# Optimization experiments

Hardware: AMD Instinct MI355X
Metric: run time of the kernel (lower is better)

## Reference

```python
import jax, jax.numpy as jnp
import numpy as np

EPSILON = 0.05
SINKHORN_ITERS = 3
TEMP = 0.1
PROB_RATIO = 1.0
LAMBD = 15.0
MU = 1.0
NU = 1.0
GAMMA = 0.2

B, D, K = 16384, 512, 2048


def setup_inputs() -> dict:
    key = jax.random.key(0)
    k1, k2, k3 = jax.random.split(key, 3)
    z_1 = jax.random.normal(k1, (B, D), dtype=jnp.float32)
    z_2 = jax.random.normal(k2, (B, D), dtype=jnp.float32)
    W = jax.random.normal(k3, (K, D), dtype=jnp.float32) * (1.0 / np.sqrt(D))
    return {"z_1": z_1, "z_2": z_2, "W": W}


def _compute_v(z):
    # unbiased variance over batch dim, matching torch.var default
    var = jnp.var(z, axis=0, ddof=1)
    return jnp.mean(jnp.maximum(0.0, GAMMA - jnp.sqrt(var + 1e-8)))


def _compute_c(z):
    n, d = z.shape
    zc = z - jnp.mean(z, axis=0, keepdims=True)
    C = (zc.T @ zc) / (n - 1)  # [d, d] unbiased covariance (torch.cov)
    off = C - jnp.diag(jnp.diag(C))
    return jnp.sum(off * off) / d


def _l2norm(z):
    return z / jnp.clip(jnp.linalg.norm(z, axis=-1, keepdims=True), 1e-12)


def _sinkhorn(out):
    # out: [B, K] raw logits (no grad path)
    b, k = out.shape
    Q = jnp.exp(out / EPSILON).T  # [K, B]
    Q = Q / jnp.sum(Q)
    for _ in range(SINKHORN_ITERS):
        Q = Q / (jnp.sum(Q, axis=1, keepdims=True) * k)
        Q = Q / (jnp.sum(Q, axis=0, keepdims=True) * b)
    Q = Q * b
    return Q.T  # [B, K]


def reference(z_1, z_2, W):
    v_z1 = _compute_v(z_1)
    v_z2 = _compute_v(z_2)
    c_z1 = _compute_c(z_1)
    c_z2 = _compute_c(z_2)

    z1n = _l2norm(z_1)
    z2n = _l2norm(z_2)
    logits_1 = z1n @ W.T  # [B, K]
    logits_2 = z2n @ W.T

    tgt_w_1 = jax.lax.stop_gradient(logits_1 * PROB_RATIO + logits_2 * (1 - PROB_RATIO))
    tgt_w_2 = jax.lax.stop_gradient(logits_2 * PROB_RATIO + logits_1 * (1 - PROB_RATIO))
    tgt_probs_1 = _sinkhorn(tgt_w_1)
    tgt_probs_2 = _sinkhorn(tgt_w_2)

    l1 = logits_1 / TEMP
    l2 = logits_2 / TEMP
    lp1 = jax.nn.log_softmax(l1, axis=1)
    lp2 = jax.nn.log_softmax(l2, axis=1)

    loss_ce = -0.5 * (jnp.mean(jnp.sum(tgt_probs_1 * lp2, axis=1))
                      + jnp.mean(jnp.sum(tgt_probs_2 * lp1, axis=1)))
    loss_var = v_z1 + v_z2
    loss_cov = c_z1 + c_z2
    loss = LAMBD * loss_ce + MU * loss_var + NU * loss_cov

    # diagnostics (no-grad in original)
    logits = jnp.concatenate([l1, l2], axis=0)  # [2B, K]
    k_idx = jnp.argmax(logits, axis=-1)
    hard_probs = jnp.zeros((K,), logits.dtype).at[k_idx].add(1.0) / logits.shape[0]
    code_perplexity = jnp.exp(-jnp.sum(hard_probs * jnp.log(hard_probs + 1e-7)))
    avg_probs = jnp.mean(jax.nn.softmax(logits, axis=-1), axis=0)
    prob_perplexity = jnp.exp(-jnp.sum(avg_probs * jnp.log(avg_probs + 1e-7)))
    acc_1 = jnp.mean((jnp.argmax(l1, axis=1) == jnp.argmax(tgt_probs_2, axis=1)).astype(jnp.float32))
    acc_2 = jnp.mean((jnp.argmax(l2, axis=1) == jnp.argmax(tgt_probs_1, axis=1)).astype(jnp.float32))
    acc = 0.5 * (acc_1 + acc_2)

    return (loss, loss_ce, loss_var, loss_cov, code_perplexity, prob_perplexity, acc)
```

## Files before the change

### kernel.cpp

```cpp
#include <hip/hip_runtime.h>
#include <hip/hip_bf16.h>

#define B_N 16384
#define D_N 512
#define K_N 2048

typedef __attribute__((ext_vector_type(8))) short bf16x8;
typedef __attribute__((ext_vector_type(4))) float f32x4;
typedef __attribute__((ext_vector_type(4))) unsigned short u16x4;
typedef unsigned short u16;

__device__ __forceinline__ float bf2f(short s) {
  return __builtin_bit_cast(float, ((unsigned)(u16)s) << 16);
}
__device__ __forceinline__ u16 f2bf(float x) {
  return __builtin_bit_cast(u16, __float2bfloat16(x));
}
__device__ __forceinline__ float wred_sum(float v) {
#pragma unroll
  for (int o = 32; o; o >>= 1) v += __shfl_down(v, o, 64);
  return v;
}

__device__ __forceinline__ void gld16(const u16* g, const u16* l) {
  __builtin_amdgcn_global_load_lds((const __attribute__((address_space(1))) void*)g,
                                   (__attribute__((address_space(3))) void*)l, 16, 0, 0);
}

__global__ __launch_bounds__(256) void k_rownorm(const float* __restrict__ z1,
                                                 const float* __restrict__ z2,
                                                 u16* __restrict__ zn1, u16* __restrict__ zn2,
                                                 u16* __restrict__ zb1, u16* __restrict__ zb2) {
  int wid = threadIdx.x >> 6, lane = threadIdx.x & 63;
  int row = blockIdx.x * 4 + wid;
  const float* z; u16 *zn, *zb; int r;
  if (row < B_N) { z = z1; zn = zn1; zb = zb1; r = row; }
  else { z = z2; zn = zn2; zb = zb2; r = row - B_N; }
  const float4* zr = (const float4*)(z + (size_t)r * D_N);
  float4 va = zr[lane], vb = zr[lane + 64];
  float ss = va.x*va.x + va.y*va.y + va.z*va.z + va.w*va.w
           + vb.x*vb.x + vb.y*vb.y + vb.z*vb.z + vb.w*vb.w;
#pragma unroll
  for (int o = 32; o; o >>= 1) ss += __shfl_xor(ss, o, 64);
  float inv = 1.0f / fmaxf(sqrtf(ss), 1e-12f);
  u16x4 pa = {f2bf(va.x), f2bf(va.y), f2bf(va.z), f2bf(va.w)};
  u16x4 pb = {f2bf(vb.x), f2bf(vb.y), f2bf(vb.z), f2bf(vb.w)};
  u16x4 na = {f2bf(va.x*inv), f2bf(va.y*inv), f2bf(va.z*inv), f2bf(va.w*inv)};
  u16x4 nb = {f2bf(vb.x*inv), f2bf(vb.y*inv), f2bf(vb.z*inv), f2bf(vb.w*inv)};
  ((u16x4*)(zb + (size_t)r * D_N))[lane] = pa;
  ((u16x4*)(zb + (size_t)r * D_N))[lane + 64] = pb;
  ((u16x4*)(zn + (size_t)r * D_N))[lane] = na;
  ((u16x4*)(zn + (size_t)r * D_N))[lane + 64] = nb;
}

__global__ __launch_bounds__(256) void k_convW(const float* __restrict__ W,
                                               u16* __restrict__ Wb) {
  size_t base = ((size_t)blockIdx.x * 256 + threadIdx.x) * 8;
#pragma unroll
  for (int j = 0; j < 8; j++) Wb[base + j] = f2bf(W[base + j]);
}

__global__ __launch_bounds__(512) void k_colstats(const u16* __restrict__ zb1,
                                                  const u16* __restrict__ zb2,
                                                  float* __restrict__ csum,
                                                  float* __restrict__ csumsq) {
  int zi = blockIdx.z;
  const u16* z = zi ? zb2 : zb1;
  __shared__ float s1[512], s2[512];
  int t = threadIdx.y * 64 + threadIdx.x;
  s1[t] = 0.f; s2[t] = 0.f;
  __syncthreads();
  int c0 = threadIdx.x * 8;
  float a[8], a2[8];
#pragma unroll
  for (int e = 0; e < 8; e++) { a[e] = 0.f; a2[e] = 0.f; }
  for (int u = 0; u < 16; u++) {
    int r = blockIdx.y * 128 + threadIdx.y + 8 * u;
    bf16x8 v = *(const bf16x8*)&z[(size_t)r * D_N + c0];
#pragma unroll
    for (int e = 0; e < 8; e++) { float x = bf2f(v[e]); a[e] += x; a2[e] += x * x; }
  }
#pragma unroll
  for (int e = 0; e < 8; e++) {
    atomicAdd(&s1[c0 + e], a[e]);
    atomicAdd(&s2[c0 + e], a2[e]);
  }
  __syncthreads();
  atomicAdd(&csum[zi * D_N + t], s1[t]);
  atomicAdd(&csumsq[zi * D_N + t], s2[t]);
}

__global__ __launch_bounds__(256) void k_vloss(const float* __restrict__ csum,
                                               const float* __restrict__ csumsq,
                                               float* __restrict__ scal) {
  int idx = blockIdx.x * 256 + threadIdx.x;
  float s = csum[idx], sq = csumsq[idx];
  float mean = s * (1.0f / (float)B_N);
  float var = (sq - (float)B_N * mean * mean) * (1.0f / (float)(B_N - 1));
  float term = fmaxf(0.f, 0.2f - sqrtf(var + 1e-8f));
  term = wred_sum(term);
  __shared__ float sw[4];
  if ((threadIdx.x & 63) == 0) sw[threadIdx.x >> 6] = term;
  __syncthreads();
  if (threadIdx.x == 0) atomicAdd(&scal[0], sw[0] + sw[1] + sw[2] + sw[3]);
}

__global__ __launch_bounds__(256) void k_gram(const u16* __restrict__ zb1,
                                              const u16* __restrict__ zb2,
                                              float* __restrict__ Gpart) {
  int zi = blockIdx.z >> 4, chunk = blockIdx.z & 15;
  const u16* z = zi ? zb2 : zb1;
  int ti = 0, xx = blockIdx.x;
  while (xx >= 8 - ti) { xx -= 8 - ti; ti++; }
  int tj = ti + xx;
  int i0 = ti * 64, j0 = tj * 64;
  __shared__ u16 lA[64][32], lB[64][32];
  int t = threadIdx.x, wid = t >> 6, lane = t & 63;
  int br = t & 31, fg = t >> 5;
  f32x4 acc[4];
#pragma unroll
  for (int q = 0; q < 4; q++) acc[q] = (f32x4){0.f, 0.f, 0.f, 0.f};
  for (int bb = 0; bb < 1024; bb += 32) {
    size_t rb = ((size_t)chunk * 1024 + bb + br) * D_N;
    bf16x8 va = *(const bf16x8*)&z[rb + i0 + fg * 8];
    bf16x8 vb = *(const bf16x8*)&z[rb + j0 + fg * 8];
#pragma unroll
    for (int e = 0; e < 8; e++) {
      lA[fg * 8 + e][br] = (u16)va[e];
      lB[fg * 8 + e][br] = (u16)vb[e];
    }
    __syncthreads();
    int m = lane & 15, q = lane >> 4;
    bf16x8 a = *(const bf16x8*)&lA[16 * wid + m][8 * q];
#pragma unroll
    for (int tt = 0; tt < 4; tt++) {
      bf16x8 b = *(const bf16x8*)&lB[16 * tt + m][8 * q];
      acc[tt] = __builtin_amdgcn_mfma_f32_16x16x32_bf16(a, b, acc[tt], 0, 0, 0);
    }
    __syncthreads();
  }
  float* gp = Gpart + (((size_t)zi * 16 + chunk) * 36 + blockIdx.x) * 4096;
  int n = lane & 15, q = lane >> 4;
#pragma unroll
  for (int tt = 0; tt < 4; tt++)
#pragma unroll
    for (int r = 0; r < 4; r++)
      gp[(16 * wid + q * 4 + r) * 64 + 16 * tt + n] = acc[tt][r];
}

__global__ __launch_bounds__(256) void k_covreduce(const float* __restrict__ Gpart,
                                                   const float* __restrict__ csum,
                                                   float* __restrict__ scal) {
  int zi = blockIdx.y;
  int tile = blockIdx.x >> 4, part = blockIdx.x & 15;
  int ti = 0, xx = tile;
  while (xx >= 8 - ti) { xx -= 8 - ti; ti++; }
  int tj = ti + xx;
  int idx = part * 256 + threadIdx.x;
  int li = idx >> 6, lj = idx & 63;
  int i = ti * 64 + li, j = tj * 64 + lj;
  float g = 0.f;
#pragma unroll
  for (int c = 0; c < 16; c++)
    g += Gpart[(((size_t)zi * 16 + c) * 36 + tile) * 4096 + idx];
  float mi = csum[zi * D_N + i] * (1.0f / (float)B_N);
  float mj = csum[zi * D_N + j] * (1.0f / (float)B_N);
  float C = (g - (float)B_N * mi * mj) * (1.0f / (float)(B_N - 1));
  float wgt = (ti == tj) ? ((li == lj) ? 0.f : 1.f) : 2.f;
  float v = wgt * C * C;
  v = wred_sum(v);
  __shared__ float sw[4];
  if ((threadIdx.x & 63) == 0) sw[threadIdx.x >> 6] = v;
  __syncthreads();
  if (threadIdx.x == 0) atomicAdd(&scal[1], sw[0] + sw[1] + sw[2] + sw[3]);
}

__global__ __launch_bounds__(256) void k_logits(const u16* __restrict__ zn1,
                                                const u16* __restrict__ zn2,
                                                const u16* __restrict__ Wb,
                                                u16* __restrict__ L1, u16* __restrict__ L2,
                                                float* __restrict__ rowsum) {
  int zi = blockIdx.z;
  const u16* A = zi ? zn2 : zn1;
  u16* Lout = zi ? L2 : L1;
  int b0 = blockIdx.x * 128, k0 = blockIdx.y * 128;
  __shared__ u16 lA[128 * 32], lB[128 * 32];
  int t = threadIdx.x, lane = t & 63, wid = t >> 6;
  int wm = wid >> 1, wn = wid & 1;
  f32x4 acc[4][4];
#pragma unroll
  for (int i = 0; i < 4; i++)
#pragma unroll
    for (int j = 0; j < 4; j++) acc[i][j] = (f32x4){0.f, 0.f, 0.f, 0.f};
  int row0 = t >> 2, seg0 = (t & 3) * 8;
  int ldsoff = (t & 192) * 16;
  for (int d0 = 0; d0 < D_N; d0 += 32) {
    gld16(A + (size_t)(b0 + row0) * D_N + d0 + seg0, (const u16*)((const char*)lA + ldsoff));
    gld16(A + (size_t)(b0 + 64 + row0) * D_N + d0 + seg0, (const u16*)((const char*)lA + 4096 + ldsoff));
    gld16(Wb + (size_t)(k0 + row0) * D_N + d0 + seg0, (const u16*)((const char*)lB + ldsoff));
    gld16(Wb + (size_t)(k0 + 64 + row0) * D_N + d0 + seg0, (const u16*)((const char*)lB + 4096 + ldsoff));
    __syncthreads();
    bf16x8 af[4], bfr[4];
#pragma unroll
    for (int i = 0; i < 4; i++)
      af[i] = *(const bf16x8*)&lA[(wm * 64 + i * 16 + (lane & 15)) * 32 + (lane >> 4) * 8];
#pragma unroll
    for (int j = 0; j < 4; j++)
      bfr[j] = *(const bf16x8*)&lB[(wn * 64 + j * 16 + (lane & 15)) * 32 + (lane >> 4) * 8];
#pragma unroll
    for (int i = 0; i < 4; i++)
#pragma unroll
      for (int j = 0; j < 4; j++)
        acc[i][j] = __builtin_amdgcn_mfma_f32_16x16x32_bf16(af[i], bfr[j], acc[i][j], 0, 0, 0);
    __syncthreads();
  }
  int cq = lane >> 4, cn = lane & 15;
  float rpart[4] = {0.f, 0.f, 0.f, 0.f};
#pragma unroll
  for (int i = 0; i < 4; i++)
#pragma unroll
    for (int j = 0; j < 4; j++)
#pragma unroll
      for (int r = 0; r < 4; r++) {
        u16 h = f2bf(acc[i][j][r]);
        int gb = b0 + wm * 64 + i * 16 + cq * 4 + r;
        int gk = k0 + wn * 64 + j * 16 + cn;
        Lout[(size_t)gb * K_N + gk] = h;
        rpart[j] += __expf(20.0f * bf2f((short)h));
      }
  float* red = (float*)lA;
  if (t < 128) red[t] = 0.f;
  __syncthreads();
#pragma unroll
  for (int j = 0; j < 4; j++) atomicAdd(&red[wn * 64 + j * 16 + cn], rpart[j]);
  __syncthreads();
  if (t < 128) atomicAdd(&rowsum[(size_t)zi * 3 * K_N + k0 + t], red[t]);
}

__global__ __launch_bounds__(256) void k_sink(const u16* __restrict__ L1,
                                              const u16* __restrict__ L2,
                                              float* __restrict__ rowsum, int it) {
  int zi = blockIdx.y;
  const u16* L = zi ? L2 : L1;
  const float* rs_in = rowsum + ((size_t)zi * 3 + it) * K_N;
  float* rs_out = rowsum + ((size_t)zi * 3 + it + 1) * K_N;
  __shared__ float pm[K_N];
  int t = threadIdx.x, lane = t & 63, wid = t >> 6;
  for (int k = t; k < K_N; k += 256) pm[k] = 0.f;
  float rv[32];
#pragma unroll
  for (int jj = 0; jj < 4; jj++) {
    const float4* p = (const float4*)&rs_in[jj * 512 + lane * 8];
    float4 x = p[0], y = p[1];
    rv[jj*8+0] = 1.0f / ((float)K_N * x.x); rv[jj*8+1] = 1.0f / ((float)K_N * x.y);
    rv[jj*8+2] = 1.0f / ((float)K_N * x.z); rv[jj*8+3] = 1.0f / ((float)K_N * x.w);
    rv[jj*8+4] = 1.0f / ((float)K_N * y.x); rv[jj*8+5] = 1.0f / ((float)K_N * y.y);
    rv[jj*8+6] = 1.0f / ((float)K_N * y.z); rv[jj*8+7] = 1.0f / ((float)K_N * y.w);
  }
  __syncthreads();
  float racc[32];
#pragma unroll
  for (int q = 0; q < 32; q++) racc[q] = 0.f;
  int w = blockIdx.x * 4 + wid;
  for (int rr = 0; rr < 8; rr++) {
    int b = w * 8 + rr;
    float ex[32];
    float c = 0.f;
#pragma unroll
    for (int jj = 0; jj < 4; jj++) {
      bf16x8 v = *(const bf16x8*)&L[(size_t)b * K_N + jj * 512 + lane * 8];
#pragma unroll
      for (int e = 0; e < 8; e++) {
        float E = __expf(20.0f * bf2f(v[e]));
        ex[jj * 8 + e] = E;
        c += E * rv[jj * 8 + e];
      }
    }
#pragma unroll
    for (int o = 32; o; o >>= 1) c += __shfl_xor(c, o, 64);
    float cb = 1.0f / ((float)B_N * c);
#pragma unroll
    for (int q = 0; q < 32; q++) racc[q] += ex[q] * cb;
  }
#pragma unroll
  for (int q = 0; q < 32; q++)
    atomicAdd(&pm[(q >> 3) * 512 + lane * 8 + (q & 7)], racc[q]);
  __syncthreads();
  for (int k = t; k < K_N; k += 256) atomicAdd(&rs_out[k], pm[k]);
}

__global__ __launch_bounds__(256) void k_final(const u16* __restrict__ L1,
                                               const u16* __restrict__ L2,
                                               const float* __restrict__ rowsum,
                                               float* __restrict__ probsum,
                                               int* __restrict__ counts,
                                               float* __restrict__ scal) {
  __shared__ float r1s[K_N], r2s[K_N], pmerge[K_N];
  const float* rs1 = rowsum + 2 * K_N;
  const float* rs2 = rowsum + 5 * K_N;
  int t = threadIdx.x, lane = t & 63, wid = t >> 6;
  for (int k = t; k < K_N; k += 256) {
    r1s[k] = 1.0f / ((float)K_N * rs1[k]);
    r2s[k] = 1.0f / ((float)K_N * rs2[k]);
    pmerge[k] = 0.f;
  }
  __syncthreads();
  float pacc[32];
#pragma unroll
  for (int q = 0; q < 32; q++) pacc[q] = 0.f;
  float ce_acc = 0.f; int acc_cnt = 0;
  int w = blockIdx.x * 4 + wid;
  for (int rr = 0; rr < 4; rr++) {
    int b = w * 4 + rr;
    float t1v[32], t2v[32];
    float sE1 = 0, sE2 = 0, d12 = 0, d21 = 0, Z1 = 0, Z2 = 0;
    float m1v = -1e30f, m2v = -1e30f, a1v = -1e30f, a2v = -1e30f;
    int m1i = 0, m2i = 0, a1i = 0, a2i = 0;
#pragma unroll
    for (int jj = 0; jj < 4; jj++) {
      bf16x8 v1 = *(const bf16x8*)&L1[(size_t)b * K_N + jj * 512 + lane * 8];
      bf16x8 v2 = *(const bf16x8*)&L2[(size_t)b * K_N + jj * 512 + lane * 8];
#pragma unroll
      for (int e = 0; e < 8; e++) {
        int k = jj * 512 + lane * 8 + e;
        float x1 = bf2f(v1[e]), x2 = bf2f(v2[e]);
        float t1 = __expf(10.0f * x1), t2 = __expf(10.0f * x2);
        t1v[jj * 8 + e] = t1; t2v[jj * 8 + e] = t2;
        float e1 = t1 * t1 * r1s[k], e2 = t2 * t2 * r2s[k];
        sE1 += e1; sE2 += e2;
        d12 += e1 * x2; d21 += e2 * x1;
        Z1 += t1; Z2 += t2;
        if (x1 > m1v) { m1v = x1; m1i = k; }
        if (x2 > m2v) { m2v = x2; m2i = k; }
        if (e1 > a1v) { a1v = e1; a1i = k; }
        if (e2 > a2v) { a2v = e2; a2i = k; }
      }
    }
#pragma unroll
    for (int o = 32; o; o >>= 1) {
      sE1 += __shfl_xor(sE1, o, 64);
      sE2 += __shfl_xor(sE2, o, 64);
      d12 += __shfl_xor(d12, o, 64);
      d21 += __shfl_xor(d21, o, 64);
      Z1 += __shfl_xor(Z1, o, 64);
      Z2 += __shfl_xor(Z2, o, 64);
      float ov; int oi;
      ov = __shfl_xor(m1v, o, 64); oi = __shfl_xor(m1i, o, 64);
      if (ov > m1v || (ov == m1v && oi < m1i)) { m1v = ov; m1i = oi; }
      ov = __shfl_xor(m2v, o, 64); oi = __shfl_xor(m2i, o, 64);
      if (ov > m2v || (ov == m2v && oi < m2i)) { m2v = ov; m2i = oi; }
      ov = __shfl_xor(a1v, o, 64); oi = __shfl_xor(a1i, o, 64);
      if (ov > a1v || (ov == a1v && oi < a1i)) { a1v = ov; a1i = oi; }
      ov = __shfl_xor(a2v, o, 64); oi = __shfl_xor(a2i, o, 64);
      if (ov > a2v || (ov == a2v && oi < a2i)) { a2v = ov; a2i = oi; }
    }
    float invc1 = 1.0f / sE1, invc2 = 1.0f / sE2;
    float lZ1 = __logf(Z1), lZ2 = __logf(Z2);
    ce_acc += (10.0f * d12) * invc1 - lZ2 + (10.0f * d21) * invc2 - lZ1;
    acc_cnt += (m1i == a2i) + (m2i == a1i);
    if (lane == 0) { atomicAdd(&counts[m1i], 1); atomicAdd(&counts[m2i], 1); }
    float iZ1 = 1.0f / Z1, iZ2 = 1.0f / Z2;
#pragma unroll
    for (int q = 0; q < 32; q++)
      pacc[q] += t1v[q] * iZ1 + t2v[q] * iZ2;
  }
  if (lane == 0) {
    atomicAdd(&scal[2], ce_acc);
    atomicAdd(&scal[3], (float)acc_cnt);
  }
#pragma unroll
  for (int q = 0; q < 32; q++) {
    int k = (q >> 3) * 512 + lane * 8 + (q & 7);
    atomicAdd(&pmerge[k], pacc[q]);
  }
  __syncthreads();
  for (int k = t; k < K_N; k += 256) atomicAdd(&probsum[k], pmerge[k]);
}

__global__ __launch_bounds__(256) void k_combine(const float* __restrict__ scal,
                                                 const float* __restrict__ probsum,
                                                 const int* __restrict__ counts,
                                                 float* __restrict__ out) {
  int t = threadIdx.x;
  float ec = 0.f, ep = 0.f;
  for (int k = t; k < K_N; k += 256) {
    float p = (float)counts[k] * (1.0f / (2.0f * (float)B_N));
    ec += -p * __logf(p + 1e-7f);
    float q = probsum[k] * (1.0f / (2.0f * (float)B_N));
    ep += -q * __logf(q + 1e-7f);
  }
  ec = wred_sum(ec);
  ep = wred_sum(ep);
  __shared__ float se[4], sp[4];
  if ((t & 63) == 0) { se[t >> 6] = ec; sp[t >> 6] = ep; }
  __syncthreads();
  if (t == 0) {
    float tec = se[0] + se[1] + se[2] + se[3];
    float tep = sp[0] + sp[1] + sp[2] + sp[3];
    float ce = -0.5f * scal[2] * (1.0f / (float)B_N);
    float lvar = scal[0] * (1.0f / (float)D_N);
    float lcov = scal[1] * (1.0f / (float)D_N);
    float acc = scal[3] * (1.0f / (2.0f * (float)B_N));
    out[0] = 15.0f * ce + lvar + lcov;
    out[1] = ce;
    out[2] = lvar;
    out[3] = lcov;
    out[4] = __expf(tec);
    out[5] = __expf(tep);
    out[6] = acc;
  }
}

extern "C" void kernel_launch(void* const* d_in, const int* in_sizes, int n_in,
                              void* d_out, int out_size, void* d_ws, size_t ws_size,
                              hipStream_t stream) {
  (void)in_sizes; (void)n_in; (void)out_size; (void)ws_size;
  const float* z1 = (const float*)d_in[0];
  const float* z2 = (const float*)d_in[1];
  const float* W = (const float*)d_in[2];

  char* w = (char*)d_ws;
  size_t off = 0;
  auto take = [&](size_t b) -> void* {
    void* p = w + off;
    off = (off + b + 255) & ~(size_t)255;
    return p;
  };
  float* rowsum = (float*)take(2 * 3 * K_N * 4);
  float* csum = (float*)take(2 * D_N * 4);
  float* csumsq = (float*)take(2 * D_N * 4);
  float* probsum = (float*)take(K_N * 4);
  int* counts = (int*)take(K_N * 4);
  float* scal = (float*)take(64);
  size_t zero_bytes = off;
  u16* zn1 = (u16*)take((size_t)B_N * D_N * 2);
  u16* zn2 = (u16*)take((size_t)B_N * D_N * 2);
  u16* Wb = (u16*)take((size_t)K_N * D_N * 2);
  u16* L1 = (u16*)take((size_t)B_N * K_N * 2);
  u16* L2 = (u16*)take((size_t)B_N * K_N * 2);
  float* Gpart = (float*)take((size_t)2 * 16 * 36 * 4096 * 4);
  u16* zb1 = L1;
  u16* zb2 = L1 + (size_t)B_N * D_N;

  hipMemsetAsync(d_ws, 0, zero_bytes, stream);

  k_rownorm<<<8192, 256, 0, stream>>>(z1, z2, zn1, zn2, zb1, zb2);
  k_convW<<<512, 256, 0, stream>>>(W, Wb);
  k_colstats<<<dim3(1, 128, 2), dim3(64, 8), 0, stream>>>(zb1, zb2, csum, csumsq);
  k_vloss<<<4, 256, 0, stream>>>(csum, csumsq, scal);
  k_gram<<<dim3(36, 1, 32), 256, 0, stream>>>(zb1, zb2, Gpart);
  k_covreduce<<<dim3(36 * 16, 2), 256, 0, stream>>>(Gpart, csum, scal);
  k_logits<<<dim3(128, 16, 2), 256, 0, stream>>>(zn1, zn2, Wb, L1, L2, rowsum);
  k_sink<<<dim3(512, 2), 256, 0, stream>>>(L1, L2, rowsum, 0);
  k_sink<<<dim3(512, 2), 256, 0, stream>>>(L1, L2, rowsum, 1);
  k_final<<<1024, 256, 0, stream>>>(L1, L2, rowsum, probsum, counts, scal);
  k_combine<<<1, 256, 0, stream>>>(scal, probsum, counts, (float*)d_out);
}
```

Before: 591.9 us.

## Cut register pressure and LDS conflicts in sinkhorn and final reduction kernels

k_sink and k_final now process fewer rows per wave, and their grids are doubled to compensate. k_final loads all bf16 logits up front and recomputes the exps for the probability sum instead of holding two 32-float arrays in registers. Each of the four argmax value/index pairs is packed into one unsigned key (masked float bits plus reversed index), so it reduces with a single integer max instead of compare-and-select shuffles. LDS accumulation uses a lane-contiguous layout to avoid bank conflicts, and r1s/r2s are read as float4. The packed argmax drops low mantissa bits and compares on exp values, so near-ties may resolve differently from the reference. The grid change also doubles the number of global atomic merges.

```diff
diff --git a/kernel.cpp b/kernel.cpp
--- a/kernel.cpp
+++ b/kernel.cpp
@@ -15,6 +15,9 @@
 }
 __device__ __forceinline__ u16 f2bf(float x) {
   return __builtin_bit_cast(u16, __float2bfloat16(x));
+}
+__device__ __forceinline__ unsigned fbits(float x) {
+  return __builtin_bit_cast(unsigned, x);
 }
 __device__ __forceinline__ float wred_sum(float v) {
 #pragma unroll
@@ -262,8 +265,8 @@
 #pragma unroll
   for (int q = 0; q < 32; q++) racc[q] = 0.f;
   int w = blockIdx.x * 4 + wid;
-  for (int rr = 0; rr < 8; rr++) {
-    int b = w * 8 + rr;
+  for (int rr = 0; rr < 4; rr++) {
+    int b = w * 4 + rr;
     float ex[32];
     float c = 0.f;
 #pragma unroll
@@ -284,9 +287,10 @@
   }
 #pragma unroll
   for (int q = 0; q < 32; q++)
-    atomicAdd(&pm[(q >> 3) * 512 + lane * 8 + (q & 7)], racc[q]);
-  __syncthreads();
-  for (int k = t; k < K_N; k += 256) atomicAdd(&rs_out[k], pm[k]);
+    atomicAdd(&pm[(q & 7) * 256 + (q >> 3) * 64 + lane], racc[q]);
+  __syncthreads();
+  for (int k = t; k < K_N; k += 256)
+    atomicAdd(&rs_out[k], pm[(k & 7) * 256 + (k >> 3)]);
 }
 
 __global__ __launch_bounds__(256) void k_final(const u16* __restrict__ L1,
@@ -310,30 +314,37 @@
   for (int q = 0; q < 32; q++) pacc[q] = 0.f;
   float ce_acc = 0.f; int acc_cnt = 0;
   int w = blockIdx.x * 4 + wid;
-  for (int rr = 0; rr < 4; rr++) {
-    int b = w * 4 + rr;
-    float t1v[32], t2v[32];
+  for (int rr = 0; rr < 2; rr++) {
+    int b = w * 2 + rr;
+    bf16x8 v1[4], v2[4];
+#pragma unroll
+    for (int jj = 0; jj < 4; jj++) {
+      v1[jj] = *(const bf16x8*)&L1[(size_t)b * K_N + jj * 512 + lane * 8];
+      v2[jj] = *(const bf16x8*)&L2[(size_t)b * K_N + jj * 512 + lane * 8];
+    }
     float sE1 = 0, sE2 = 0, d12 = 0, d21 = 0, Z1 = 0, Z2 = 0;
-    float m1v = -1e30f, m2v = -1e30f, a1v = -1e30f, a2v = -1e30f;
-    int m1i = 0, m2i = 0, a1i = 0, a2i = 0;
+    unsigned um1 = 0, um2 = 0, ua1 = 0, ua2 = 0;
 #pragma unroll
     for (int jj = 0; jj < 4; jj++) {
-      bf16x8 v1 = *(const bf16x8*)&L1[(size_t)b * K_N + jj * 512 + lane * 8];
-      bf16x8 v2 = *(const bf16x8*)&L2[(size_t)b * K_N + jj * 512 + lane * 8];
+      const float4* rp1 = (const float4*)&r1s[jj * 512 + lane * 8];
+      float4 r1a = rp1[0], r1b = rp1[1];
+      const float4* rp2 = (const float4*)&r2s[jj * 512 + lane * 8];
+      float4 r2a = rp2[0], r2b = rp2[1];
+      float rv1[8] = {r1a.x, r1a.y, r1a.z, r1a.w, r1b.x, r1b.y, r1b.z, r1b.w};
+      float rv2[8] = {r2a.x, r2a.y, r2a.z, r2a.w, r2b.x, r2b.y, r2b.z, r2b.w};
 #pragma unroll
       for (int e = 0; e < 8; e++) {
-        int k = jj * 512 + lane * 8 + e;
-        float x1 = bf2f(v1[e]), x2 = bf2f(v2[e]);
+        unsigned ik = 2047u - (unsigned)(jj * 512 + lane * 8 + e);
+        float x1 = bf2f(v1[jj][e]), x2 = bf2f(v2[jj][e]);
         float t1 = __expf(10.0f * x1), t2 = __expf(10.0f * x2);
-        t1v[jj * 8 + e] = t1; t2v[jj * 8 + e] = t2;
-        float e1 = t1 * t1 * r1s[k], e2 = t2 * t2 * r2s[k];
+        float e1 = t1 * t1 * rv1[e], e2 = t2 * t2 * rv2[e];
         sE1 += e1; sE2 += e2;
         d12 += e1 * x2; d21 += e2 * x1;
         Z1 += t1; Z2 += t2;
-        if (x1 > m1v) { m1v = x1; m1i = k; }
-        if (x2 > m2v) { m2v = x2; m2i = k; }
-        if (e1 > a1v) { a1v = e1; a1i = k; }
-        if (e2 > a2v) { a2v = e2; a2i = k; }
+        um1 = max(um1, (fbits(t1) & 0xFFFFF800u) | ik);
+        um2 = max(um2, (fbits(t2) & 0xFFFFF800u) | ik);
+        ua1 = max(ua1, (fbits(e1) & 0xFFFFF800u) | ik);
+        ua2 = max(ua2, (fbits(e2) & 0xFFFFF800u) | ik);
       }
     }
 #pragma unroll
@@ -344,16 +355,15 @@
       d21 += __shfl_xor(d21, o, 64);
       Z1 += __shfl_xor(Z1, o, 64);
       Z2 += __shfl_xor(Z2, o, 64);
-      float ov; int oi;
-      ov = __shfl_xor(m1v, o, 64); oi = __shfl_xor(m1i, o, 64);
-      if (ov > m1v || (ov == m1v && oi < m1i)) { m1v = ov; m1i = oi; }
-      ov = __shfl_xor(m2v, o, 64); oi = __shfl_xor(m2i, o, 64);
-      if (ov > m2v || (ov == m2v && oi < m2i)) { m2v = ov; m2i = oi; }
-      ov = __shfl_xor(a1v, o, 64); oi = __shfl_xor(a1i, o, 64);
-      if (ov > a1v || (ov == a1v && oi < a1i)) { a1v = ov; a1i = oi; }
-      ov = __shfl_xor(a2v, o, 64); oi = __shfl_xor(a2i, o, 64);
-      if (ov > a2v || (ov == a2v && oi < a2i)) { a2v = ov; a2i = oi; }
-    }
+      um1 = max(um1, (unsigned)__shfl_xor((int)um1, o, 64));
+      um2 = max(um2, (unsigned)__shfl_xor((int)um2, o, 64));
+      ua1 = max(ua1, (unsigned)__shfl_xor((int)ua1, o, 64));
+      ua2 = max(ua2, (unsigned)__shfl_xor((int)ua2, o, 64));
+    }
+    int m1i = 2047 - (int)(um1 & 2047u);
+    int m2i = 2047 - (int)(um2 & 2047u);
+    int a1i = 2047 - (int)(ua1 & 2047u);
+    int a2i = 2047 - (int)(ua2 & 2047u);
     float invc1 = 1.0f / sE1, invc2 = 1.0f / sE2;
     float lZ1 = __logf(Z1), lZ2 = __logf(Z2);
     ce_acc += (10.0f * d12) * invc1 - lZ2 + (10.0f * d21) * invc2 - lZ1;
@@ -361,18 +371,20 @@
     if (lane == 0) { atomicAdd(&counts[m1i], 1); atomicAdd(&counts[m2i], 1); }
     float iZ1 = 1.0f / Z1, iZ2 = 1.0f / Z2;
 #pragma unroll
-    for (int q = 0; q < 32; q++)
-      pacc[q] += t1v[q] * iZ1 + t2v[q] * iZ2;
+    for (int jj = 0; jj < 4; jj++)
+#pragma unroll
+      for (int e = 0; e < 8; e++) {
+        float x1 = bf2f(v1[jj][e]), x2 = bf2f(v2[jj][e]);
+        pacc[jj * 8 + e] += __expf(10.0f * x1) * iZ1 + __expf(10.0f * x2) * iZ2;
+      }
   }
   if (lane == 0) {
     atomicAdd(&scal[2], ce_acc);
     atomicAdd(&scal[3], (float)acc_cnt);
   }
 #pragma unroll
-  for (int q = 0; q < 32; q++) {
-    int k = (q >> 3) * 512 + lane * 8 + (q & 7);
-    atomicAdd(&pmerge[k], pacc[q]);
-  }
+  for (int q = 0; q < 32; q++)
+    atomicAdd(&pmerge[(q & 7) * 256 + (q >> 3) * 64 + lane], pacc[q]);
   __syncthreads();
   for (int k = t; k < K_N; k += 256) atomicAdd(&probsum[k], pmerge[k]);
 }
@@ -451,8 +463,8 @@
   k_gram<<<dim3(36, 1, 32), 256, 0, stream>>>(zb1, zb2, Gpart);
   k_covreduce<<<dim3(36 * 16, 2), 256, 0, stream>>>(Gpart, csum, scal);
   k_logits<<<dim3(128, 16, 2), 256, 0, stream>>>(zn1, zn2, Wb, L1, L2, rowsum);
-  k_sink<<<dim3(512, 2), 256, 0, stream>>>(L1, L2, rowsum, 0);
-  k_sink<<<dim3(512, 2), 256, 0, stream>>>(L1, L2, rowsum, 1);
-  k_final<<<1024, 256, 0, stream>>>(L1, L2, rowsum, probsum, counts, scal);
+  k_sink<<<dim3(1024, 2), 256, 0, stream>>>(L1, L2, rowsum, 0);
+  k_sink<<<dim3(1024, 2), 256, 0, stream>>>(L1, L2, rowsum, 1);
+  k_final<<<2048, 256, 0, stream>>>(L1, L2, rowsum, probsum, counts, scal);
   k_combine<<<1, 256, 0, stream>>>(scal, probsum, counts, (float*)d_out);
 }
```

After: 753.3 us. 27.3% more time.
